# Kernel optimization log

Measured on AMD Instinct MI355X. Metric: run time of the kernel, lower is better.

Reference implementation:

```python
import jax, jax.numpy as jnp
import numpy as np

NUM_HEADS = 8
NUM_GROUPS = 32
EPS = 1e-5


def setup_inputs() -> dict:
    key = jax.random.key(0)
    ks = jax.random.split(key, 3)
    B, C, H, W = 8, 512, 32, 32
    X = jax.random.normal(ks[0], (B, C, H, W), dtype=jnp.float32)
    norm_w = jnp.ones((C,), jnp.float32)
    norm_b = jnp.zeros((C,), jnp.float32)
    qkv_w = jax.random.normal(ks[1], (3 * C, C), dtype=jnp.float32) * (1.0 / np.sqrt(C))
    qkv_b = jnp.zeros((3 * C,), jnp.float32)
    proj_w = jax.random.normal(ks[2], (C, C), dtype=jnp.float32) * (1.0 / np.sqrt(C))
    proj_b = jnp.zeros((C,), jnp.float32)
    return {"X": X, "norm_w": norm_w, "norm_b": norm_b,
            "qkv_w": qkv_w, "qkv_b": qkv_b, "proj_w": proj_w, "proj_b": proj_b}


def group_norm(x, w, b):
    B, C, H, W = x.shape
    xg = x.reshape(B, NUM_GROUPS, C // NUM_GROUPS, H, W)
    mean = xg.mean(axis=(2, 3, 4), keepdims=True)
    var = xg.var(axis=(2, 3, 4), keepdims=True)
    xg = (xg - mean) * jax.lax.rsqrt(var + EPS)
    x = xg.reshape(B, C, H, W)
    return x * w[None, :, None, None] + b[None, :, None, None]


def reference(X, norm_w, norm_b, qkv_w, qkv_b, proj_w, proj_b):
    B, C, H, W = X.shape
    hd = C // NUM_HEADS  # head_dim
    residual = X
    Xn = group_norm(X, norm_w, norm_b)
    # 1x1 conv == channel matmul: [B, 3C, H, W]
    qkv = jnp.einsum('oc,bchw->bohw', qkv_w, Xn) + qkv_b[None, :, None, None]
    q, k, v = jnp.split(qkv, 3, axis=1)
    S = H * W
    q = q.reshape(B, NUM_HEADS, hd, S)
    k = k.reshape(B, NUM_HEADS, hd, S)
    v = v.reshape(B, NUM_HEADS, hd, S)
    scale = hd ** -0.5
    attn = jnp.einsum('bhdq,bhdk->bhqk', q, k) * scale  # [B,H,S,S]
    attn = jax.nn.softmax(attn, axis=-1)
    out = jnp.einsum('bhqk,bhdk->bhqd', attn, v)  # [B,H,S,hd]
    out = out.transpose(0, 1, 3, 2).reshape(B, C, H, W)
    out = jnp.einsum('oc,bchw->bohw', proj_w, out) + proj_b[None, :, None, None]
    return out + residual
```

## Files before the change

### kernel.cpp

```cpp
#include <hip/hip_runtime.h>
#include <hip/hip_bf16.h>


#define BATCH 8
#define C 512
#define S 1024
#define HEADS 8
#define OC3 1536

typedef short bf16x8 __attribute__((ext_vector_type(8)));
typedef float f32x4 __attribute__((ext_vector_type(4)));
typedef unsigned u32x2 __attribute__((ext_vector_type(2)));
typedef unsigned short u16;
typedef unsigned short u16x4 __attribute__((ext_vector_type(4)));

__device__ inline short f2bf(float x) {
    union { float f; unsigned u; } v; v.f = x;
    unsigned r = v.u + 0x7fffu + ((v.u >> 16) & 1u);
    return (short)(r >> 16);
}

__device__ inline unsigned cvt_pk_bf16(float lo, float hi) {
    unsigned r;
    asm("v_cvt_pk_bf16_f32 %0, %1, %2" : "=v"(r) : "v"(lo), "v"(hi));
    return r;
}

__device__ inline void gload_lds16(const u16* g, short* l) {
    __builtin_amdgcn_global_load_lds(
        (const __attribute__((address_space(1))) unsigned int*)g,
        (__attribute__((address_space(3))) unsigned int*)l, 16, 0, 0);
}

__global__ __launch_bounds__(512) void prep_kernel(
    const float* __restrict__ X, const float* __restrict__ nw,
    const float* __restrict__ nb, u16* __restrict__ Xn_t,
    const float* __restrict__ wq, const float* __restrict__ wp,
    u16* __restrict__ oq, u16* __restrict__ op)
{
    const int tid = threadIdx.x;
    if (blockIdx.x >= 256) {
        int j = (blockIdx.x - 256) * 512 + tid;
        const float* w; u16* o;
        if (j < 98304) { w = wq; o = oq; }
        else           { w = wp; o = op; j -= 98304; }
        f32x4 a = *(const f32x4*)(w + (size_t)j * 8);
        f32x4 b = *(const f32x4*)(w + (size_t)j * 8 + 4);
        bf16x8 r;
        #pragma unroll
        for (int k = 0; k < 4; ++k) { r[k] = f2bf(a[k]); r[4 + k] = f2bf(b[k]); }
        *(bf16x8*)(o + (size_t)j * 8) = r;
        return;
    }
    const int blk = blockIdx.x;
    const int bi = blk >> 5, g = blk & 31;
    __shared__ __attribute__((aligned(16))) float T[16][1032];
    __shared__ float red[16];
    __shared__ float sh_mr[2];

    const float* Xg = X + ((size_t)bi * C + g * 16) * S;
    float s = 0.f, ss = 0.f;
    #pragma unroll
    for (int r = 0; r < 8; ++r) {
        int idx4 = r * 512 + tid;
        f32x4 v = *(const f32x4*)(Xg + (size_t)idx4 * 4);
        int c = idx4 >> 8, sp = (idx4 * 4) & 1023;
        *(f32x4*)&T[c][sp] = v;
        s  += v[0] + v[1] + v[2] + v[3];
        ss += v[0]*v[0] + v[1]*v[1] + v[2]*v[2] + v[3]*v[3];
    }
    #pragma unroll
    for (int m = 1; m <= 32; m <<= 1) {
        s += __shfl_xor(s, m); ss += __shfl_xor(ss, m);
    }
    if ((tid & 63) == 0) { red[tid >> 6] = s; red[8 + (tid >> 6)] = ss; }
    __syncthreads();
    if (tid == 0) {
        float S1 = 0.f, S2 = 0.f;
        #pragma unroll
        for (int w = 0; w < 8; ++w) { S1 += red[w]; S2 += red[8 + w]; }
        float mean = S1 * (1.f / 16384.f);
        float var  = S2 * (1.f / 16384.f) - mean * mean;
        sh_mr[0] = mean; sh_mr[1] = rsqrtf(var + 1e-5f);
    }
    __syncthreads();
    const float mean = sh_mr[0], rstd = sh_mr[1];
    float rw[16], sb[16];
    #pragma unroll
    for (int c = 0; c < 16; ++c) {
        float w = nw[g * 16 + c], b = nb[g * 16 + c];
        rw[c] = rstd * w;
        sb[c] = b - mean * rw[c];
    }
    #pragma unroll
    for (int r = 0; r < 2; ++r) {
        int sp = r * 512 + tid;
        bf16x8 o0, o1;
        #pragma unroll
        for (int c = 0; c < 8; ++c) o0[c] = f2bf(T[c][sp] * rw[c] + sb[c]);
        #pragma unroll
        for (int c = 0; c < 8; ++c) o1[c] = f2bf(T[8 + c][sp] * rw[8 + c] + sb[8 + c]);
        u16* dst = Xn_t + ((size_t)bi * S + sp) * C + g * 16;
        *(bf16x8*)dst = o0;
        *(bf16x8*)(dst + 8) = o1;
    }
}

__global__ __launch_bounds__(256) void qkv_mfma(
    const u16* __restrict__ A, const u16* __restrict__ Bt,
    const float* __restrict__ bias,
    u16* __restrict__ Qt, u16* __restrict__ Kt, u16* __restrict__ Vn)
{
    const int n0 = blockIdx.x * 128, m0 = blockIdx.y * 128;
    const int bi = blockIdx.z;
    const int tid = threadIdx.x, wave = tid >> 6, lane = tid & 63;
    const int lr = lane & 15, lg = lane >> 4;
    const int wr = wave >> 1, wc = wave & 1;

    __shared__ __attribute__((aligned(16))) short SM[3][8][1024];

    f32x4 acc[4][4];
    #pragma unroll
    for (int i = 0; i < 4; ++i)
        #pragma unroll
        for (int j = 0; j < 4; ++j) acc[i][j] = (f32x4){0.f, 0.f, 0.f, 0.f};

    const u16* aP0 = A + (size_t)(m0 + wave * 16 + lr) * C + lg * 8;
    const u16* aP1 = A + (size_t)(m0 + (wave + 4) * 16 + lr) * C + lg * 8;
    const u16* bP0 = Bt + (size_t)bi * S * C + (size_t)(n0 + wave * 16 + lr) * C + lg * 8;
    const u16* bP1 = Bt + (size_t)bi * S * C + (size_t)(n0 + (wave + 4) * 16 + lr) * C + lg * 8;

    auto STAGE = [&](int buf, int t) {
        const int k0 = t * 32;
        gload_lds16(aP0 + k0, &SM[buf][wave][0]);
        gload_lds16(aP1 + k0, &SM[buf][wave + 4][0]);
        gload_lds16(bP0 + k0, &SM[buf][wave][512]);
        gload_lds16(bP1 + k0, &SM[buf][wave + 4][512]);
    };

    STAGE(0, 0);
    STAGE(1, 1);
    asm volatile("s_waitcnt vmcnt(4)" ::: "memory");
    __builtin_amdgcn_s_barrier();
    __builtin_amdgcn_sched_barrier(0);

    #pragma unroll
    for (int kt = 0; kt < 16; ++kt) {
        const int cur = kt % 3;
        if (kt < 14) STAGE((kt + 2) % 3, kt + 2);
        bf16x8 af[4], bfr[4];
        #pragma unroll
        for (int mf = 0; mf < 4; ++mf) af[mf] = *(bf16x8*)&SM[cur][wr * 4 + mf][lane * 8];
        #pragma unroll
        for (int nf = 0; nf < 4; ++nf) bfr[nf] = *(bf16x8*)&SM[cur][wc * 4 + nf][512 + lane * 8];
        __builtin_amdgcn_s_setprio(1);
        #pragma unroll
        for (int mf = 0; mf < 4; ++mf)
            #pragma unroll
            for (int nf = 0; nf < 4; ++nf)
                acc[mf][nf] = __builtin_amdgcn_mfma_f32_16x16x32_bf16(
                    af[mf], bfr[nf], acc[mf][nf], 0, 0, 0);
        __builtin_amdgcn_s_setprio(0);
        if (kt < 15) {
            if (kt < 14) asm volatile("s_waitcnt vmcnt(4)" ::: "memory");
            else         asm volatile("s_waitcnt vmcnt(0)" ::: "memory");
            __builtin_amdgcn_s_barrier();
            __builtin_amdgcn_sched_barrier(0);
        }
    }

    const float QSCALE = 0.125f * 1.44269504088896f;
    if (m0 < 1024) {
        #pragma unroll
        for (int mf = 0; mf < 4; ++mf) {
            const int o3b = m0 + wr * 64 + mf * 16 + 4 * lg;
            float bv[4];
            #pragma unroll
            for (int i = 0; i < 4; ++i) bv[i] = bias[o3b + i];
            #pragma unroll
            for (int nf = 0; nf < 4; ++nf) {
                const int s = n0 + wc * 64 + nf * 16 + lr;
                if (m0 < 512) {
                    int h = o3b >> 6, d = o3b & 63;
                    u16x4 pk;
                    #pragma unroll
                    for (int i = 0; i < 4; ++i)
                        pk[i] = (u16)f2bf((acc[mf][nf][i] + bv[i]) * QSCALE);
                    *(u16x4*)(Qt + (((size_t)bi * 8 + h) * S + s) * 64 + d) = pk;
                } else {
                    int ok = o3b - 512;
                    int h = ok >> 6, d = ok & 63;
                    u16x4 pk;
                    #pragma unroll
                    for (int i = 0; i < 4; ++i) pk[i] = (u16)f2bf(acc[mf][nf][i] + bv[i]);
                    *(u16x4*)(Kt + (((size_t)bi * 8 + h) * S + s) * 64 + d) = pk;
                }
            }
        }
    } else {
        __syncthreads();
        short* Ts = &SM[0][0][0];
        #pragma unroll
        for (int mf = 0; mf < 4; ++mf) {
            const int orl = wr * 64 + mf * 16 + 4 * lg;
            float bv[4];
            #pragma unroll
            for (int i = 0; i < 4; ++i) bv[i] = bias[m0 + orl + i];
            #pragma unroll
            for (int nf = 0; nf < 4; ++nf) {
                const int srl = wc * 64 + nf * 16 + lr;
                #pragma unroll
                for (int i = 0; i < 4; ++i) {
                    int o = orl + i;
                    Ts[o * 128 + (srl ^ ((o & 7) << 3))] =
                        (short)f2bf(acc[mf][nf][i] + bv[i]);
                }
            }
        }
        __syncthreads();
        const int o = tid >> 1, half = (tid & 1) * 64;
        const int x = (o & 7) << 3;
        const int ov0 = m0 - 1024;
        u16* vdst = Vn + (size_t)(bi * C + ov0 + o) * S + n0 + half;
        #pragma unroll
        for (int c = 0; c < 8; ++c)
            *(bf16x8*)(vdst + 8 * c) = *(bf16x8*)&Ts[o * 128 + ((half + 8 * c) ^ x)];
    }
}

__global__ __launch_bounds__(256) void attn_mfma(
    const u16* __restrict__ Qt, const u16* __restrict__ Kt,
    const u16* __restrict__ Vn, u16* __restrict__ At)
{
    const int bh = blockIdx.x, qb = blockIdx.y;
    const int bi = bh >> 3, h = bh & 7;
    const int tid = threadIdx.x, wave = tid >> 6, lane = tid & 63;
    const int lr = lane & 15, lg = lane >> 4;
    const int q0 = qb * 128 + wave * 32;

    const u16* qt = Qt + ((size_t)bi * 8 + h) * S * 64;
    const u16* kp = Kt + ((size_t)bi * 8 + h) * S * 64;
    const u16* vp = Vn + (size_t)(bi * C + h * 64) * S;

    __shared__ __attribute__((aligned(16))) short Ks[3][4096];
    __shared__ __attribute__((aligned(16))) short Vs[3][4096];
    __shared__ __attribute__((aligned(16))) unsigned Pw[4][32 * 32];

    bf16x8 bq[2][2];
    #pragma unroll
    for (int qf = 0; qf < 2; ++qf)
        #pragma unroll
        for (int dc = 0; dc < 2; ++dc)
            bq[qf][dc] = *(const bf16x8*)(qt + (size_t)(q0 + qf * 16 + lr) * 64 + dc * 32 + lg * 8);

    float mrun[2] = {-1e30f, -1e30f}, lrun[2] = {0.f, 0.f};
    f32x4 acc[4][2];
    #pragma unroll
    for (int df = 0; df < 4; ++df)
        #pragma unroll
        for (int qf = 0; qf < 2; ++qf) acc[df][qf] = (f32x4){0.f, 0.f, 0.f, 0.f};

    auto STAGE = [&](int buf, int kt0) {
        #pragma unroll
        for (int p = 0; p < 2; ++p) {
            int idx = p * 256 + tid;
            int r = idx >> 3, cs = (idx & 7) ^ (r & 7);
            short* ldsK = &Ks[buf][(p * 256 + (wave << 6)) * 8];
            short* ldsV = &Vs[buf][(p * 256 + (wave << 6)) * 8];
            gload_lds16(kp + (size_t)(kt0 + r) * 64 + cs * 8, ldsK);
            gload_lds16(vp + (size_t)r * S + kt0 + cs * 8, ldsV);
        }
    };

    unsigned* pwb = &Pw[wave][0];
    const int swz = (lr & 7) << 2;

    STAGE(0, 0);
    STAGE(1, 64);
    asm volatile("s_waitcnt vmcnt(4)" ::: "memory");
    __builtin_amdgcn_s_barrier();
    __builtin_amdgcn_sched_barrier(0);

    #pragma unroll
    for (int kt = 0; kt < 16; ++kt) {
        const int cur = kt % 3;
        if (kt < 14) STAGE((kt + 2) % 3, (kt + 2) * 64);

        f32x4 sc[4][2];
        __builtin_amdgcn_s_setprio(1);
        #pragma unroll
        for (int kf = 0; kf < 4; ++kf) {
            int rK = kf * 16 + lr;
            bf16x8 b0 = *(bf16x8*)&Ks[cur][rK * 64 + (lg ^ (rK & 7)) * 8];
            bf16x8 b1 = *(bf16x8*)&Ks[cur][rK * 64 + ((lg + 4) ^ (rK & 7)) * 8];
            #pragma unroll
            for (int qf = 0; qf < 2; ++qf) {
                f32x4 z = (f32x4){0.f, 0.f, 0.f, 0.f};
                z = __builtin_amdgcn_mfma_f32_16x16x32_bf16(b0, bq[qf][0], z, 0, 0, 0);
                sc[kf][qf] = __builtin_amdgcn_mfma_f32_16x16x32_bf16(b1, bq[qf][1], z, 0, 0, 0);
            }
        }
        __builtin_amdgcn_s_setprio(0);

        float tmax[2];
        #pragma unroll
        for (int qf = 0; qf < 2; ++qf) {
            float t = sc[0][qf][0];
            #pragma unroll
            for (int kf = 0; kf < 4; ++kf)
                #pragma unroll
                for (int i = 0; i < 4; ++i) t = fmaxf(t, sc[kf][qf][i]);
            t = fmaxf(t, __shfl_xor(t, 16));
            t = fmaxf(t, __shfl_xor(t, 32));
            tmax[qf] = t;
        }

        float grow = fmaxf(tmax[0] - mrun[0], tmax[1] - mrun[1]);
        if (!__all(grow <= 8.f)) {
            #pragma unroll
            for (int qf = 0; qf < 2; ++qf) {
                float mnew = fmaxf(mrun[qf], tmax[qf]);
                float fac = __builtin_amdgcn_exp2f(mrun[qf] - mnew);
                mrun[qf] = mnew;
                lrun[qf] *= fac;
                #pragma unroll
                for (int df = 0; df < 4; ++df) acc[df][qf] *= fac;
            }
        }

        float sum[2] = {0.f, 0.f};
        #pragma unroll
        for (int kf = 0; kf < 4; ++kf)
            #pragma unroll
            for (int qf = 0; qf < 2; ++qf)
                #pragma unroll
                for (int i = 0; i < 4; ++i) {
                    sc[kf][qf][i] = __builtin_amdgcn_exp2f(sc[kf][qf][i] - mrun[qf]);
                    sum[qf] += sc[kf][qf][i];
                }

        #pragma unroll
        for (int kf = 0; kf < 4; ++kf)
            #pragma unroll
            for (int qf = 0; qf < 2; ++qf) {
                unsigned p0 = cvt_pk_bf16(sc[kf][qf][0], sc[kf][qf][1]);
                unsigned p1 = cvt_pk_bf16(sc[kf][qf][2], sc[kf][qf][3]);
                int idx = (qf * 16 + lr) * 32 + ((8 * kf + 2 * lg) ^ swz);
                *(u32x2*)&pwb[idx] = (u32x2){p0, p1};
            }

        #pragma unroll
        for (int qf = 0; qf < 2; ++qf) {
            sum[qf] += __shfl_xor(sum[qf], 16);
            sum[qf] += __shfl_xor(sum[qf], 32);
            lrun[qf] += sum[qf];
        }

        bf16x8 pb[2][2];
        #pragma unroll
        for (int qf = 0; qf < 2; ++qf)
            #pragma unroll
            for (int c = 0; c < 2; ++c)
                pb[qf][c] = *(bf16x8*)&pwb[(qf * 16 + lr) * 32 + ((lg * 4 + 16 * c) ^ swz)];
        __builtin_amdgcn_s_setprio(1);
        #pragma unroll
        for (int df = 0; df < 4; ++df) {
            int rV = df * 16 + lr;
            bf16x8 v0 = *(bf16x8*)&Vs[cur][rV * 64 + (lg ^ (rV & 7)) * 8];
            bf16x8 v1 = *(bf16x8*)&Vs[cur][rV * 64 + ((lg + 4) ^ (rV & 7)) * 8];
            #pragma unroll
            for (int qf = 0; qf < 2; ++qf) {
                acc[df][qf] = __builtin_amdgcn_mfma_f32_16x16x32_bf16(v0, pb[qf][0], acc[df][qf], 0, 0, 0);
                acc[df][qf] = __builtin_amdgcn_mfma_f32_16x16x32_bf16(v1, pb[qf][1], acc[df][qf], 0, 0, 0);
            }
        }
        __builtin_amdgcn_s_setprio(0);

        if (kt < 15) {
            if (kt < 14) asm volatile("s_waitcnt vmcnt(4)" ::: "memory");
            else         asm volatile("s_waitcnt vmcnt(0)" ::: "memory");
            __builtin_amdgcn_s_barrier();
            __builtin_amdgcn_sched_barrier(0);
        }
    }

    #pragma unroll
    for (int qf = 0; qf < 2; ++qf) {
        float linv = 1.f / lrun[qf];
        #pragma unroll
        for (int df = 0; df < 4; ++df) {
            u16x4 pk;
            #pragma unroll
            for (int i = 0; i < 4; ++i) pk[i] = (u16)f2bf(acc[df][qf][i] * linv);
            *(u16x4*)(At + ((size_t)bi * S + q0 + qf * 16 + lr) * C + h * 64 + df * 16 + 4 * lg) = pk;
        }
    }
}

__global__ __launch_bounds__(256) void proj_mfma(
    const u16* __restrict__ A, const u16* __restrict__ Bt,
    const float* __restrict__ bias, const float* __restrict__ Xres,
    float* __restrict__ out)
{
    const int n0 = blockIdx.x * 128, m0 = blockIdx.y * 128;
    const int bi = blockIdx.z;
    const int tid = threadIdx.x, wave = tid >> 6, lane = tid & 63;
    const int lr = lane & 15, lg = lane >> 4;
    const int wr = wave >> 1, wc = wave & 1;

    __shared__ __attribute__((aligned(16))) short SM[3][8][1024];

    f32x4 acc[4][4];
    #pragma unroll
    for (int i = 0; i < 4; ++i)
        #pragma unroll
        for (int j = 0; j < 4; ++j) acc[i][j] = (f32x4){0.f, 0.f, 0.f, 0.f};

    const u16* aP0 = A + (size_t)(m0 + wave * 16 + lr) * C + lg * 8;
    const u16* aP1 = A + (size_t)(m0 + (wave + 4) * 16 + lr) * C + lg * 8;
    const u16* bP0 = Bt + (size_t)bi * S * C + (size_t)(n0 + wave * 16 + lr) * C + lg * 8;
    const u16* bP1 = Bt + (size_t)bi * S * C + (size_t)(n0 + (wave + 4) * 16 + lr) * C + lg * 8;

    auto STAGE = [&](int buf, int t) {
        const int k0 = t * 32;
        gload_lds16(aP0 + k0, &SM[buf][wave][0]);
        gload_lds16(aP1 + k0, &SM[buf][wave + 4][0]);
        gload_lds16(bP0 + k0, &SM[buf][wave][512]);
        gload_lds16(bP1 + k0, &SM[buf][wave + 4][512]);
    };

    STAGE(0, 0);
    STAGE(1, 1);
    asm volatile("s_waitcnt vmcnt(4)" ::: "memory");
    __builtin_amdgcn_s_barrier();
    __builtin_amdgcn_sched_barrier(0);

    #pragma unroll
    for (int kt = 0; kt < 16; ++kt) {
        const int cur = kt % 3;
        if (kt < 14) STAGE((kt + 2) % 3, kt + 2);
        bf16x8 af[4], bfr[4];
        #pragma unroll
        for (int mf = 0; mf < 4; ++mf) af[mf] = *(bf16x8*)&SM[cur][wr * 4 + mf][lane * 8];
        #pragma unroll
        for (int nf = 0; nf < 4; ++nf) bfr[nf] = *(bf16x8*)&SM[cur][wc * 4 + nf][512 + lane * 8];
        __builtin_amdgcn_s_setprio(1);
        #pragma unroll
        for (int mf = 0; mf < 4; ++mf)
            #pragma unroll
            for (int nf = 0; nf < 4; ++nf)
                acc[mf][nf] = __builtin_amdgcn_mfma_f32_16x16x32_bf16(
                    af[mf], bfr[nf], acc[mf][nf], 0, 0, 0);
        __builtin_amdgcn_s_setprio(0);
        if (kt < 15) {
            if (kt < 14) asm volatile("s_waitcnt vmcnt(4)" ::: "memory");
            else         asm volatile("s_waitcnt vmcnt(0)" ::: "memory");
            __builtin_amdgcn_s_barrier();
            __builtin_amdgcn_sched_barrier(0);
        }
    }

    #pragma unroll
    for (int mf = 0; mf < 4; ++mf) {
        const int ob = m0 + wr * 64 + mf * 16 + 4 * lg;
        float bv[4];
        #pragma unroll
        for (int i = 0; i < 4; ++i) bv[i] = bias[ob + i];
        #pragma unroll
        for (int nf = 0; nf < 4; ++nf) {
            const int s = n0 + wc * 64 + nf * 16 + lr;
            #pragma unroll
            for (int i = 0; i < 4; ++i) {
                size_t oi = ((size_t)bi * C + ob + i) * S + s;
                out[oi] = acc[mf][nf][i] + bv[i] + Xres[oi];
            }
        }
    }
}

extern "C" void kernel_launch(void* const* d_in, const int* in_sizes, int n_in,
                              void* d_out, int out_size, void* d_ws, size_t ws_size,
                              hipStream_t stream) {
    const float* X      = (const float*)d_in[0];
    const float* norm_w = (const float*)d_in[1];
    const float* norm_b = (const float*)d_in[2];
    const float* qkv_w  = (const float*)d_in[3];
    const float* qkv_b  = (const float*)d_in[4];
    const float* proj_w = (const float*)d_in[5];
    const float* proj_b = (const float*)d_in[6];
    float* out = (float*)d_out;

    u16* Wq_bf = (u16*)d_ws;
    u16* Wp_bf = Wq_bf + 786432;
    u16* Xn_t  = Wp_bf + 262144;
    u16* Qt    = Xn_t + 4194304;
    u16* Kt    = Qt + 4194304;
    u16* Vn    = Kt + 4194304;
    u16* At    = Vn + 4194304;

    prep_kernel<<<dim3(512), 512, 0, stream>>>(
        X, norm_w, norm_b, Xn_t, qkv_w, proj_w, Wq_bf, Wp_bf);
    qkv_mfma<<<dim3(S / 128, OC3 / 128, BATCH), 256, 0, stream>>>(
        Wq_bf, Xn_t, qkv_b, Qt, Kt, Vn);
    attn_mfma<<<dim3(64, S / 128), 256, 0, stream>>>(Qt, Kt, Vn, At);
    proj_mfma<<<dim3(S / 128, C / 128, BATCH), 256, 0, stream>>>(
        Wp_bf, At, proj_b, X, out);
}
```

Baseline: 88.52 us.

## Enlarge QKV GEMM tiles to 256x256 with 512 threads and swizzled LDS

The QKV projection GEMM moves from 128x128 tiles with 256 threads and a triple-buffered K=32 pipeline to 256x256 tiles with 512 threads, double-buffered K=64 stages, and an XOR-swizzled LDS layout. Each wave now holds 8x4 accumulator fragments, which raises data reuse per load and cuts the number of k-iterations and barriers. The grid shrinks from 768 blocks to 192 blocks. That risks poor occupancy and CU underfill on a large GPU, and register pressure rises from the larger accumulator set.

```diff
diff --git a/kernel.cpp b/kernel.cpp
--- a/kernel.cpp
+++ b/kernel.cpp
@@ -106,64 +106,85 @@
     }
 }
 
-__global__ __launch_bounds__(256) void qkv_mfma(
+__global__ __launch_bounds__(512) void qkv_mfma(
     const u16* __restrict__ A, const u16* __restrict__ Bt,
     const float* __restrict__ bias,
     u16* __restrict__ Qt, u16* __restrict__ Kt, u16* __restrict__ Vn)
 {
-    const int n0 = blockIdx.x * 128, m0 = blockIdx.y * 128;
+    const int n0 = blockIdx.x * 256, m0 = blockIdx.y * 256;
     const int bi = blockIdx.z;
     const int tid = threadIdx.x, wave = tid >> 6, lane = tid & 63;
     const int lr = lane & 15, lg = lane >> 4;
-    const int wr = wave >> 1, wc = wave & 1;
-
-    __shared__ __attribute__((aligned(16))) short SM[3][8][1024];
-
-    f32x4 acc[4][4];
-    #pragma unroll
-    for (int i = 0; i < 4; ++i)
+    const int wr = wave >> 2, wc = wave & 3;
+
+    __shared__ __attribute__((aligned(16))) short SM[65536];
+
+    f32x4 acc[8][4];
+    #pragma unroll
+    for (int i = 0; i < 8; ++i)
         #pragma unroll
         for (int j = 0; j < 4; ++j) acc[i][j] = (f32x4){0.f, 0.f, 0.f, 0.f};
 
-    const u16* aP0 = A + (size_t)(m0 + wave * 16 + lr) * C + lg * 8;
-    const u16* aP1 = A + (size_t)(m0 + (wave + 4) * 16 + lr) * C + lg * 8;
-    const u16* bP0 = Bt + (size_t)bi * S * C + (size_t)(n0 + wave * 16 + lr) * C + lg * 8;
-    const u16* bP1 = Bt + (size_t)bi * S * C + (size_t)(n0 + (wave + 4) * 16 + lr) * C + lg * 8;
+    const int l8 = lane >> 3;
+    const int c16 = (lane & 7) ^ l8;
+    const u16* aBase = A + (size_t)(m0 + wave * 32 + l8) * C + c16 * 8;
+    const u16* bBase = Bt + (size_t)bi * S * C + (size_t)(n0 + wave * 32 + l8) * C + c16 * 8;
 
     auto STAGE = [&](int buf, int t) {
-        const int k0 = t * 32;
-        gload_lds16(aP0 + k0, &SM[buf][wave][0]);
-        gload_lds16(aP1 + k0, &SM[buf][wave + 4][0]);
-        gload_lds16(bP0 + k0, &SM[buf][wave][512]);
-        gload_lds16(bP1 + k0, &SM[buf][wave + 4][512]);
+        const int k0 = t * 64;
+        short* as = SM + buf * 16384 + wave * 2048;
+        short* bs = SM + 32768 + buf * 16384 + wave * 2048;
+        #pragma unroll
+        for (int j = 0; j < 4; ++j) {
+            gload_lds16(aBase + k0 + (size_t)j * 8 * C, as + j * 512);
+            gload_lds16(bBase + k0 + (size_t)j * 8 * C, bs + j * 512);
+        }
     };
 
     STAGE(0, 0);
-    STAGE(1, 1);
-    asm volatile("s_waitcnt vmcnt(4)" ::: "memory");
+    asm volatile("s_waitcnt vmcnt(0)" ::: "memory");
     __builtin_amdgcn_s_barrier();
     __builtin_amdgcn_sched_barrier(0);
 
     #pragma unroll
-    for (int kt = 0; kt < 16; ++kt) {
-        const int cur = kt % 3;
-        if (kt < 14) STAGE((kt + 2) % 3, kt + 2);
-        bf16x8 af[4], bfr[4];
-        #pragma unroll
-        for (int mf = 0; mf < 4; ++mf) af[mf] = *(bf16x8*)&SM[cur][wr * 4 + mf][lane * 8];
-        #pragma unroll
-        for (int nf = 0; nf < 4; ++nf) bfr[nf] = *(bf16x8*)&SM[cur][wc * 4 + nf][512 + lane * 8];
-        __builtin_amdgcn_s_setprio(1);
-        #pragma unroll
-        for (int mf = 0; mf < 4; ++mf)
-            #pragma unroll
-            for (int nf = 0; nf < 4; ++nf)
-                acc[mf][nf] = __builtin_amdgcn_mfma_f32_16x16x32_bf16(
-                    af[mf], bfr[nf], acc[mf][nf], 0, 0, 0);
-        __builtin_amdgcn_s_setprio(0);
-        if (kt < 15) {
-            if (kt < 14) asm volatile("s_waitcnt vmcnt(4)" ::: "memory");
-            else         asm volatile("s_waitcnt vmcnt(0)" ::: "memory");
+    for (int kt = 0; kt < 8; ++kt) {
+        const int cur = kt & 1;
+        if (kt < 7) STAGE(cur ^ 1, kt + 1);
+        const short* as = SM + cur * 16384;
+        const short* bs = SM + 32768 + cur * 16384;
+
+        bf16x8 bfr[4][2];
+        #pragma unroll
+        for (int nf = 0; nf < 4; ++nf) {
+            int r = wc * 64 + nf * 16 + lr;
+            #pragma unroll
+            for (int h = 0; h < 2; ++h)
+                bfr[nf][h] = *(bf16x8*)&bs[r * 64 + (((h << 2) + lg) ^ (r & 7)) * 8];
+        }
+        #pragma unroll
+        for (int half = 0; half < 2; ++half) {
+            bf16x8 afr[4][2];
+            #pragma unroll
+            for (int mf = 0; mf < 4; ++mf) {
+                int r = wr * 128 + (half * 4 + mf) * 16 + lr;
+                #pragma unroll
+                for (int h = 0; h < 2; ++h)
+                    afr[mf][h] = *(bf16x8*)&as[r * 64 + (((h << 2) + lg) ^ (r & 7)) * 8];
+            }
+            __builtin_amdgcn_s_setprio(1);
+            #pragma unroll
+            for (int mf = 0; mf < 4; ++mf)
+                #pragma unroll
+                for (int nf = 0; nf < 4; ++nf) {
+                    acc[half * 4 + mf][nf] = __builtin_amdgcn_mfma_f32_16x16x32_bf16(
+                        afr[mf][0], bfr[nf][0], acc[half * 4 + mf][nf], 0, 0, 0);
+                    acc[half * 4 + mf][nf] = __builtin_amdgcn_mfma_f32_16x16x32_bf16(
+                        afr[mf][1], bfr[nf][1], acc[half * 4 + mf][nf], 0, 0, 0);
+                }
+            __builtin_amdgcn_s_setprio(0);
+        }
+        if (kt < 7) {
+            asm volatile("s_waitcnt vmcnt(0)" ::: "memory");
             __builtin_amdgcn_s_barrier();
             __builtin_amdgcn_sched_barrier(0);
         }
@@ -172,8 +193,8 @@
     const float QSCALE = 0.125f * 1.44269504088896f;
     if (m0 < 1024) {
         #pragma unroll
-        for (int mf = 0; mf < 4; ++mf) {
-            const int o3b = m0 + wr * 64 + mf * 16 + 4 * lg;
+        for (int mf = 0; mf < 8; ++mf) {
+            const int o3b = m0 + wr * 128 + mf * 16 + 4 * lg;
             float bv[4];
             #pragma unroll
             for (int i = 0; i < 4; ++i) bv[i] = bias[o3b + i];
@@ -199,10 +220,9 @@
         }
     } else {
         __syncthreads();
-        short* Ts = &SM[0][0][0];
-        #pragma unroll
-        for (int mf = 0; mf < 4; ++mf) {
-            const int orl = wr * 64 + mf * 16 + 4 * lg;
+        #pragma unroll
+        for (int mf = 0; mf < 8; ++mf) {
+            const int orl = wr * 128 + mf * 16 + 4 * lg;
             float bv[4];
             #pragma unroll
             for (int i = 0; i < 4; ++i) bv[i] = bias[m0 + orl + i];
@@ -212,19 +232,20 @@
                 #pragma unroll
                 for (int i = 0; i < 4; ++i) {
                     int o = orl + i;
-                    Ts[o * 128 + (srl ^ ((o & 7) << 3))] =
+                    SM[o * 256 + (srl ^ ((o & 7) << 3))] =
                         (short)f2bf(acc[mf][nf][i] + bv[i]);
                 }
             }
         }
         __syncthreads();
-        const int o = tid >> 1, half = (tid & 1) * 64;
-        const int x = (o & 7) << 3;
+        const int o = tid >> 1, half = (tid & 1) * 128;
         const int ov0 = m0 - 1024;
         u16* vdst = Vn + (size_t)(bi * C + ov0 + o) * S + n0 + half;
         #pragma unroll
-        for (int c = 0; c < 8; ++c)
-            *(bf16x8*)(vdst + 8 * c) = *(bf16x8*)&Ts[o * 128 + ((half + 8 * c) ^ x)];
+        for (int c = 0; c < 16; ++c) {
+            int sl = half + 8 * c;
+            *(bf16x8*)(vdst + 8 * c) = *(bf16x8*)&SM[o * 256 + (sl ^ ((o & 7) << 3))];
+        }
     }
 }
 
@@ -500,7 +521,7 @@
 
     prep_kernel<<<dim3(512), 512, 0, stream>>>(
         X, norm_w, norm_b, Xn_t, qkv_w, proj_w, Wq_bf, Wp_bf);
-    qkv_mfma<<<dim3(S / 128, OC3 / 128, BATCH), 256, 0, stream>>>(
+    qkv_mfma<<<dim3(S / 256, OC3 / 256, BATCH), 512, 0, stream>>>(
         Wq_bf, Xn_t, qkv_b, Qt, Kt, Vn);
     attn_mfma<<<dim3(64, S / 128), 256, 0, stream>>>(Qt, Kt, Vn, At);
     proj_mfma<<<dim3(S / 128, C / 128, BATCH), 256, 0, stream>>>(
```

After: 81.32 us. -8.1%, faster.
